# Optimization experiments

Measured on AMD Instinct MI355X. Metric: run time of the kernel, lower is better.

## Reference

```python
import jax, jax.numpy as jnp
import numpy as np

B, C, H, W = 8, 256, 160, 160

def setup_inputs() -> dict:
    key = jax.random.key(0)
    kx, kw, kh = jax.random.split(key, 3)
    x = jax.random.normal(kx, (B, C, H, W), dtype=jnp.float32)
    # kaiming_normal fan_in, relu -> std = sqrt(2/fan_in)
    fcw_w = jax.random.normal(kw, (1, W), dtype=jnp.float32) * np.float32(np.sqrt(2.0 / W))
    fch_w = jax.random.normal(kh, (1, H), dtype=jnp.float32) * np.float32(np.sqrt(2.0 / H))
    fcw_b = jnp.zeros((1,), dtype=jnp.float32)
    fch_b = jnp.zeros((1,), dtype=jnp.float32)
    return {"x": x, "fcw_w": fcw_w, "fcw_b": fcw_b, "fch_w": fch_w, "fch_b": fch_b}

def reference(x, fcw_w, fcw_b, fch_w, fch_b):
    b, c, h, w = x.shape
    xr = x.reshape(b * c, h, w)                                   # (n,h,w)
    # fc_w: Linear(w,1) then softmax over h (dim=1 of (n,h,1))
    alpha = jax.nn.softmax(jnp.einsum('nhw,w->nh', xr, fcw_w[0]) + fcw_b[0], axis=1)  # (n,h)
    # repeat+bmm == broadcasting a softmax-weighted row-sum to every row:
    # x_c[n,i,:] = sum_h alpha[n,h] * x[n,h,:]  (same for all i)
    row = jnp.einsum('nh,nhw->nw', alpha, xr)                      # (n,w)
    # fc_h on x_c^T (n,w,h): each h-column of x_c^T equals row, so the
    # Linear(h,1) reduces to row * sum(fch_w) + bias (identical math)
    beta = jax.nn.softmax(row * jnp.sum(fch_w[0]) + fch_b[0], axis=1)  # (n,w)
    # second repeat+bmm collapses to a scalar per (b,c): sum_w beta*row
    s = jnp.einsum('nw,nw->n', beta, row)                          # (n,)
    out = jnp.broadcast_to(s[:, None, None], (b * c, h, w)).reshape(b, c, h, w)
    return out
```

## Files before the change

### kernel.cpp

```cpp
#include <hip/hip_runtime.h>


#define HH 160
#define WW 160
#define NPLANE (HH * WW)
#define BLOCK 320
#define RPT 20
#define QN 40
#define PSTR 41

typedef float f32x4 __attribute__((ext_vector_type(4)));

__global__ void __launch_bounds__(BLOCK, 8) sa1_kernel(
    const float* __restrict__ x,
    const float* __restrict__ fcw_w,
    const float* __restrict__ fch_w,
    float* __restrict__ out)
{
    const int n = blockIdx.x;
    const int t = threadIdx.x;
    const int q = t % QN;
    const int v = t / QN;

    __shared__ float pbuf[HH * PSTR];
    __shared__ float larr[HH];
    __shared__ float sc[4];

    const float* xp = x + (size_t)n * NPLANE;
    float*       op = out + (size_t)n * NPLANE;

    const float4 ww = *(const float4*)(fcw_w + 4 * q);

#pragma unroll
    for (int r = 0; r < RPT; ++r) {
        const float4 x4 = *(const float4*)(xp + (size_t)(v * RPT + r) * WW + 4 * q);
        pbuf[(v * RPT + r) * PSTR + q] =
            x4.x * ww.x + x4.y * ww.y + x4.z * ww.z + x4.w * ww.w;
    }
    __syncthreads();

    if (t < HH) {
        const float* pr = pbuf + t * PSTR;
        float s0 = 0.f, s1 = 0.f, s2 = 0.f, s3 = 0.f;
#pragma unroll
        for (int qq = 0; qq < QN; qq += 4) {
            s0 += pr[qq]; s1 += pr[qq + 1]; s2 += pr[qq + 2]; s3 += pr[qq + 3];
        }
        larr[t] = (s0 + s1) + (s2 + s3);
    }
    __syncthreads();

    if (t < 32) {
        float lv[5];
#pragma unroll
        for (int j = 0; j < 5; ++j) lv[j] = larr[t + 32 * j];
        float m = lv[0];
#pragma unroll
        for (int j = 1; j < 5; ++j) m = fmaxf(m, lv[j]);
#pragma unroll
        for (int off = 16; off >= 1; off >>= 1)
            m = fmaxf(m, __shfl_down(m, off, 32));
        m = __shfl(m, 0, 32);
        float z = 0.f;
#pragma unroll
        for (int j = 0; j < 5; ++j) z += __expf(lv[j] - m);
#pragma unroll
        for (int off = 16; off >= 1; off >>= 1)
            z += __shfl_down(z, off, 32);
        if (t == 0) { sc[0] = m; sc[1] = z; }
    } else if (t >= 64 && t < 96) {
        const int u = t - 64;
        float s = 0.f;
#pragma unroll
        for (int j = 0; j < 5; ++j) s += fch_w[u + 32 * j];
#pragma unroll
        for (int off = 16; off >= 1; off >>= 1)
            s += __shfl_down(s, off, 32);
        if (u == 0) sc[2] = s;
    }
    __syncthreads();

    if (t < HH) larr[t] = __expf(larr[t] - sc[0]);
    __syncthreads();

    float4 rp = make_float4(0.f, 0.f, 0.f, 0.f);
#pragma unroll
    for (int r = 0; r < RPT; ++r) {
        const float4 x4 = *(const float4*)(xp + (size_t)(v * RPT + r) * WW + 4 * q);
        const float a = larr[v * RPT + r];
        rp.x += a * x4.x; rp.y += a * x4.y;
        rp.z += a * x4.z; rp.w += a * x4.w;
    }
    pbuf[v * WW + 4 * q + 0] = rp.x;
    pbuf[v * WW + 4 * q + 1] = rp.y;
    pbuf[v * WW + 4 * q + 2] = rp.z;
    pbuf[v * WW + 4 * q + 3] = rp.w;
    __syncthreads();

    if (t < WW) {
        float rs = 0.f;
#pragma unroll
        for (int vv = 0; vv < 8; ++vv) rs += pbuf[vv * WW + t];
        larr[t] = rs / sc[1];
    }
    __syncthreads();

    if (t < 32) {
        const float S = sc[2];
        float rv[5], bl[5];
#pragma unroll
        for (int j = 0; j < 5; ++j) { rv[j] = larr[t + 32 * j]; bl[j] = rv[j] * S; }
        float mb = bl[0];
#pragma unroll
        for (int j = 1; j < 5; ++j) mb = fmaxf(mb, bl[j]);
#pragma unroll
        for (int off = 16; off >= 1; off >>= 1)
            mb = fmaxf(mb, __shfl_down(mb, off, 32));
        mb = __shfl(mb, 0, 32);
        float zb = 0.f, sd = 0.f;
#pragma unroll
        for (int j = 0; j < 5; ++j) {
            float e = __expf(bl[j] - mb);
            zb += e; sd += e * rv[j];
        }
#pragma unroll
        for (int off = 16; off >= 1; off >>= 1) {
            zb += __shfl_down(zb, off, 32);
            sd += __shfl_down(sd, off, 32);
        }
        if (t == 0) sc[3] = sd / zb;
    }
    __syncthreads();

    const float sv = sc[3];
    const f32x4 o = { sv, sv, sv, sv };
#pragma unroll
    for (int r = 0; r < RPT; ++r)
        __builtin_nontemporal_store(o, (f32x4*)(op + (size_t)(v * RPT + r) * WW + 4 * q));
}

extern "C" void kernel_launch(void* const* d_in, const int* in_sizes, int n_in,
                              void* d_out, int out_size, void* d_ws, size_t ws_size,
                              hipStream_t stream) {
    const float* x     = (const float*)d_in[0];
    const float* fcw_w = (const float*)d_in[1];
    const float* fch_w = (const float*)d_in[3];
    float* out = (float*)d_out;

    const int nplanes = 8 * 256;
    sa1_kernel<<<nplanes, BLOCK, 0, stream>>>(x, fcw_w, fch_w, out);
}
```

Before: 402.6 us.

## Fuse softmax and weighted row-sum into single pass with online softmax

Replaces the two-pass scheme, which read each plane of x twice, with a chunked online-softmax pass. Each thread keeps its rows in registers, computes logits chunk by chunk, and rescales a running max, normalizer and weighted accumulator. Per-group partial maxima and normalizers are then merged across the 8 row groups. This removes the second global read of x at the cost of more barriers per chunk and extra exp rescaling, and the output stores switch from nontemporal to plain stores.

```diff
diff --git a/kernel.cpp b/kernel.cpp
--- a/kernel.cpp
+++ b/kernel.cpp
@@ -7,9 +7,9 @@
 #define BLOCK 320
 #define RPT 20
 #define QN 40
+#define CHUNK 5
+#define NCHUNK 4
 #define PSTR 41
-
-typedef float f32x4 __attribute__((ext_vector_type(4)));
 
 __global__ void __launch_bounds__(BLOCK, 8) sa1_kernel(
     const float* __restrict__ x,
@@ -24,6 +24,7 @@
 
     __shared__ float pbuf[HH * PSTR];
     __shared__ float larr[HH];
+    __shared__ float gm[8], gz[8];
     __shared__ float sc[4];
 
     const float* xp = x + (size_t)n * NPLANE;
@@ -31,44 +32,7 @@
 
     const float4 ww = *(const float4*)(fcw_w + 4 * q);
 
-#pragma unroll
-    for (int r = 0; r < RPT; ++r) {
-        const float4 x4 = *(const float4*)(xp + (size_t)(v * RPT + r) * WW + 4 * q);
-        pbuf[(v * RPT + r) * PSTR + q] =
-            x4.x * ww.x + x4.y * ww.y + x4.z * ww.z + x4.w * ww.w;
-    }
-    __syncthreads();
-
-    if (t < HH) {
-        const float* pr = pbuf + t * PSTR;
-        float s0 = 0.f, s1 = 0.f, s2 = 0.f, s3 = 0.f;
-#pragma unroll
-        for (int qq = 0; qq < QN; qq += 4) {
-            s0 += pr[qq]; s1 += pr[qq + 1]; s2 += pr[qq + 2]; s3 += pr[qq + 3];
-        }
-        larr[t] = (s0 + s1) + (s2 + s3);
-    }
-    __syncthreads();
-
-    if (t < 32) {
-        float lv[5];
-#pragma unroll
-        for (int j = 0; j < 5; ++j) lv[j] = larr[t + 32 * j];
-        float m = lv[0];
-#pragma unroll
-        for (int j = 1; j < 5; ++j) m = fmaxf(m, lv[j]);
-#pragma unroll
-        for (int off = 16; off >= 1; off >>= 1)
-            m = fmaxf(m, __shfl_down(m, off, 32));
-        m = __shfl(m, 0, 32);
-        float z = 0.f;
-#pragma unroll
-        for (int j = 0; j < 5; ++j) z += __expf(lv[j] - m);
-#pragma unroll
-        for (int off = 16; off >= 1; off >>= 1)
-            z += __shfl_down(z, off, 32);
-        if (t == 0) { sc[0] = m; sc[1] = z; }
-    } else if (t >= 64 && t < 96) {
+    if (t >= 64 && t < 96) {
         const int u = t - 64;
         float s = 0.f;
 #pragma unroll
@@ -78,30 +42,77 @@
             s += __shfl_down(s, off, 32);
         if (u == 0) sc[2] = s;
     }
+
+    float  m_run = -3.0e38f;
+    float  Z_run = 0.f;
+    float4 acc   = make_float4(0.f, 0.f, 0.f, 0.f);
+
+    for (int c = 0; c < NCHUNK; ++c) {
+        float4 x4[CHUNK];
+#pragma unroll
+        for (int r = 0; r < CHUNK; ++r) {
+            const int h = v * RPT + c * CHUNK + r;
+            x4[r] = *(const float4*)(xp + (size_t)h * WW + 4 * q);
+            pbuf[h * PSTR + q] =
+                x4[r].x * ww.x + x4[r].y * ww.y + x4[r].z * ww.z + x4[r].w * ww.w;
+        }
+        __syncthreads();
+
+        const int tt = t - 64 * c;
+        if (tt >= 0 && tt < QN) {
+            const int h = RPT * (tt / CHUNK) + c * CHUNK + (tt % CHUNK);
+            const float* pr = pbuf + h * PSTR;
+            float s0 = 0.f, s1 = 0.f, s2 = 0.f, s3 = 0.f;
+#pragma unroll
+            for (int qq = 0; qq < QN; qq += 4) {
+                s0 += pr[qq]; s1 += pr[qq + 1]; s2 += pr[qq + 2]; s3 += pr[qq + 3];
+            }
+            larr[h] = (s0 + s1) + (s2 + s3);
+        }
+        __syncthreads();
+
+        float lv[CHUNK];
+        float mc = -3.0e38f;
+#pragma unroll
+        for (int r = 0; r < CHUNK; ++r) {
+            lv[r] = larr[v * RPT + c * CHUNK + r];
+            mc = fmaxf(mc, lv[r]);
+        }
+        const float m_new = fmaxf(m_run, mc);
+        const float scale = __expf(m_run - m_new);
+        Z_run *= scale;
+        acc.x *= scale; acc.y *= scale; acc.z *= scale; acc.w *= scale;
+#pragma unroll
+        for (int r = 0; r < CHUNK; ++r) {
+            const float a = __expf(lv[r] - m_new);
+            Z_run += a;
+            acc.x += a * x4[r].x; acc.y += a * x4[r].y;
+            acc.z += a * x4[r].z; acc.w += a * x4[r].w;
+        }
+        m_run = m_new;
+    }
+
+    if (q == 0) { gm[v] = m_run; gz[v] = Z_run; }
     __syncthreads();
 
-    if (t < HH) larr[t] = __expf(larr[t] - sc[0]);
-    __syncthreads();
-
-    float4 rp = make_float4(0.f, 0.f, 0.f, 0.f);
+    float m_g = gm[0];
 #pragma unroll
-    for (int r = 0; r < RPT; ++r) {
-        const float4 x4 = *(const float4*)(xp + (size_t)(v * RPT + r) * WW + 4 * q);
-        const float a = larr[v * RPT + r];
-        rp.x += a * x4.x; rp.y += a * x4.y;
-        rp.z += a * x4.z; rp.w += a * x4.w;
-    }
-    pbuf[v * WW + 4 * q + 0] = rp.x;
-    pbuf[v * WW + 4 * q + 1] = rp.y;
-    pbuf[v * WW + 4 * q + 2] = rp.z;
-    pbuf[v * WW + 4 * q + 3] = rp.w;
+    for (int j = 1; j < 8; ++j) m_g = fmaxf(m_g, gm[j]);
+    const float f = __expf(m_run - m_g);
+    pbuf[v * WW + 4 * q + 0] = f * acc.x;
+    pbuf[v * WW + 4 * q + 1] = f * acc.y;
+    pbuf[v * WW + 4 * q + 2] = f * acc.z;
+    pbuf[v * WW + 4 * q + 3] = f * acc.w;
     __syncthreads();
 
     if (t < WW) {
         float rs = 0.f;
 #pragma unroll
         for (int vv = 0; vv < 8; ++vv) rs += pbuf[vv * WW + t];
-        larr[t] = rs / sc[1];
+        float zg = 0.f;
+#pragma unroll
+        for (int j = 0; j < 8; ++j) zg += __expf(gm[j] - m_g) * gz[j];
+        larr[t] = rs / zg;
     }
     __syncthreads();
 
@@ -133,10 +144,10 @@
     __syncthreads();
 
     const float sv = sc[3];
-    const f32x4 o = { sv, sv, sv, sv };
+    const float4 o = make_float4(sv, sv, sv, sv);
 #pragma unroll
     for (int r = 0; r < RPT; ++r)
-        __builtin_nontemporal_store(o, (f32x4*)(op + (size_t)(v * RPT + r) * WW + 4 * q));
+        *(float4*)(op + (size_t)(v * RPT + r) * WW + 4 * q) = o;
 }
 
 extern "C" void kernel_launch(void* const* d_in, const int* in_sizes, int n_in,
```

Measured after the change: 426.8 us. 6.0% more time.
